# Kernel tuning notes

Hardware: AMD Instinct MI355X
Metric: run time of the kernel (lower is better)

Reference implementation:

```python
import jax, jax.numpy as jnp
import numpy as np

BATCH = 256
SEQ_LEN = 96
PRED_LEN = 96
ENC_IN = 321
D_MODEL = 512


def setup_inputs() -> dict:
    key = jax.random.key(0)
    ks = jax.random.split(key, 7)
    s = 1.0 / np.sqrt(D_MODEL)
    x_enc = jax.random.normal(ks[0], (BATCH, SEQ_LEN, ENC_IN), jnp.float32)
    Wih = jax.random.uniform(ks[1], (4 * D_MODEL, ENC_IN), jnp.float32, -s, s)
    Whh = jax.random.uniform(ks[2], (4 * D_MODEL, D_MODEL), jnp.float32, -s, s)
    bih = jax.random.uniform(ks[3], (4 * D_MODEL,), jnp.float32, -s, s)
    bhh = jax.random.uniform(ks[4], (4 * D_MODEL,), jnp.float32, -s, s)
    Wp = jax.random.uniform(ks[5], (ENC_IN, D_MODEL), jnp.float32, -s, s)
    bp = jax.random.uniform(ks[6], (ENC_IN,), jnp.float32, -s, s)
    return {"x_enc": x_enc, "Wih": Wih, "Whh": Whh, "bih": bih, "bhh": bhh, "Wp": Wp, "bp": bp}


def _lstm_step(h, c, xt, Wih, Whh, bih, bhh):
    # PyTorch LSTM gate layout: [i, f, g, o]
    g = xt @ Wih.T + h @ Whh.T + (bih + bhh)  # (B, 4*D)
    i, f, gg, o = jnp.split(g, 4, axis=-1)
    c = jax.nn.sigmoid(f) * c + jax.nn.sigmoid(i) * jnp.tanh(gg)
    h = jax.nn.sigmoid(o) * jnp.tanh(c)
    return h, c


def reference(x_enc, Wih, Whh, bih, bhh, Wp, bp):
    # Instance norm over time (use_norm=True); means detached as in torch
    means = jax.lax.stop_gradient(jnp.mean(x_enc, axis=1, keepdims=True))
    xc = x_enc - means
    stdev = jnp.sqrt(jnp.var(xc, axis=1, keepdims=True) + 1e-5)
    x = xc / stdev

    B = x.shape[0]
    h0 = jnp.zeros((B, D_MODEL), x.dtype)
    c0 = jnp.zeros((B, D_MODEL), x.dtype)

    def enc_step(carry, xt):
        h, c = carry
        h, c = _lstm_step(h, c, xt, Wih, Whh, bih, bhh)
        return (h, c), None

    (h, c), _ = jax.lax.scan(enc_step, (h0, c0), jnp.swapaxes(x, 0, 1))

    def dec_step(carry, _):
        h, c = carry
        y = h @ Wp.T + bp          # (B, ENC_IN) decoded from hidden
        h, c = _lstm_step(h, c, y, Wih, Whh, bih, bhh)
        return (h, c), y

    _, ys = jax.lax.scan(dec_step, (h, c), None, length=PRED_LEN)
    dec_out = jnp.swapaxes(ys, 0, 1)  # (B, PRED_LEN, ENC_IN)

    dec_out = dec_out * stdev[:, 0:1, :] + means[:, 0:1, :]
    return dec_out
```

## Files before the change

kernel.cpp:

```cpp
#include <hip/hip_runtime.h>
#include <hip/hip_bf16.h>
#include <math.h>

#define BB 256
#define TT 96
#define PP 96
#define CC 321
#define CP 352
#define DD 512
#define GG 2048
#define NSTEPS 191

typedef __attribute__((ext_vector_type(8))) short bf16x8;
typedef __attribute__((ext_vector_type(4))) float f32x4;
typedef __hip_bfloat16 bf16;
typedef unsigned long long u64;

__global__ void norm_kernel(const float* __restrict__ x, float* __restrict__ meanp,
                            float* __restrict__ stdp, bf16* __restrict__ xn) {
    int g = blockIdx.x * 256 + threadIdx.x;
    if (g >= BB * CC) return;
    int b = g / CC, c = g % CC;
    const float* xp = x + b * TT * CC + c;
    float s = 0.f;
    for (int t = 0; t < TT; ++t) s += xp[t * CC];
    float mu = s * (1.f / TT);
    float v = 0.f;
    for (int t = 0; t < TT; ++t) { float d0 = xp[t * CC] - mu; v += d0 * d0; }
    float sd = sqrtf(v * (1.f / TT) + 1e-5f);
    float rs = 1.f / sd;
    meanp[g] = mu;
    stdp[g] = sd;
    for (int t = 0; t < TT; ++t)
        xn[(t * BB + b) * CP + c] = __float2bfloat16((xp[t * CC] - mu) * rs);
}

__global__ void cast_pad_kernel(const float* __restrict__ src, bf16* __restrict__ dst,
                                int rows, int cols, int ldd) {
    int i = blockIdx.x * 256 + threadIdx.x;
    if (i >= rows * cols) return;
    int r = i / cols, c = i % cols;
    dst[r * ldd + c] = __float2bfloat16(src[i]);
}

__global__ void transpose_wp_kernel(const float* __restrict__ wp, bf16* __restrict__ wpt) {
    int i = blockIdx.x * 256 + threadIdx.x;
    if (i >= DD * CC) return;
    int d = i / CC, c = i % CC;
    wpt[d * CP + c] = __float2bfloat16(wp[c * DD + d]);
}

__global__ void bias_kernel(const float* __restrict__ Wih, const float* __restrict__ bih,
                            const float* __restrict__ bhh, const float* __restrict__ bp,
                            float* __restrict__ bsum, float* __restrict__ beff) {
    int j = blockIdx.x * 256 + threadIdx.x;
    if (j >= GG) return;
    float s = bih[j] + bhh[j];
    float acc = 0.f;
    const float* w = Wih + j * CC;
    for (int c = 0; c < CC; ++c) acc += w[c] * bp[c];
    bsum[j] = s;
    beff[j] = s + acc;
}

__device__ __forceinline__ void gemm_core_64x64(const bf16* A, int lda, const bf16* Bt,
                                                int ldb, int K, int m0, int n0,
                                                f32x4 acc[4]) {
    __shared__ unsigned short As[64][40];
    __shared__ unsigned short Bs[64][40];
    int tid = threadIdx.x;
    int w = tid >> 6, lane = tid & 63;
    int quad = lane >> 4, col = lane & 15;
    int lr = tid >> 2, lc = (tid & 3) * 8;
    for (int k0 = 0; k0 < K; k0 += 32) {
        __syncthreads();
        *(uint4*)&As[lr][lc] = *(const uint4*)&A[(size_t)(m0 + lr) * lda + k0 + lc];
        *(uint4*)&Bs[lr][lc] = *(const uint4*)&Bt[(size_t)(n0 + lr) * ldb + k0 + lc];
        __syncthreads();
        bf16x8 a = *(const bf16x8*)&As[w * 16 + col][quad * 8];
#pragma unroll
        for (int nt = 0; nt < 4; ++nt) {
            bf16x8 bfr = *(const bf16x8*)&Bs[nt * 16 + col][quad * 8];
            acc[nt] = __builtin_amdgcn_mfma_f32_16x16x32_bf16(a, bfr, acc[nt], 0, 0, 0);
        }
    }
}

__global__ void weff_kernel(const bf16* __restrict__ WihP, const bf16* __restrict__ WpTP,
                            const float* __restrict__ Whh, bf16* __restrict__ WeffP) {
    f32x4 acc[4] = {{0,0,0,0},{0,0,0,0},{0,0,0,0},{0,0,0,0}};
    int m0 = blockIdx.y * 64, n0 = blockIdx.x * 64;
    gemm_core_64x64(WihP, CP, WpTP, CP, CP, m0, n0, acc);
    int tid = threadIdx.x, w = tid >> 6, lane = tid & 63;
    int quad = lane >> 4, col = lane & 15;
#pragma unroll
    for (int nt = 0; nt < 4; ++nt)
#pragma unroll
        for (int r = 0; r < 4; ++r) {
            int j = m0 + w * 16 + quad * 4 + r;
            int d = n0 + nt * 16 + col;
            WeffP[j * DD + d] = __float2bfloat16(acc[nt][r] + Whh[j * DD + d]);
        }
}

__global__ void proj_kernel(const bf16* __restrict__ Hdec, const bf16* __restrict__ WpP,
                            const float* __restrict__ bp, const float* __restrict__ stdp,
                            const float* __restrict__ meanp, float* __restrict__ out) {
    f32x4 acc[4] = {{0,0,0,0},{0,0,0,0},{0,0,0,0},{0,0,0,0}};
    int m0 = blockIdx.x * 64, n0 = blockIdx.y * 64;
    gemm_core_64x64(Hdec, DD, WpP, DD, DD, m0, n0, acc);
    int tid = threadIdx.x, w = tid >> 6, lane = tid & 63;
    int quad = lane >> 4, col = lane & 15;
#pragma unroll
    for (int nt = 0; nt < 4; ++nt) {
        int c = n0 + nt * 16 + col;
        if (c >= CC) continue;
        float bpc = bp[c];
#pragma unroll
        for (int r = 0; r < 4; ++r) {
            int row = m0 + w * 16 + quad * 4 + r;
            int t = row >> 8, b = row & 255;
            float y = acc[nt][r] + bpc;
            int sc = b * CC + c;
            out[(b * PP + t) * CC + c] = y * stdp[sc] + meanp[sc];
        }
    }
}

__global__ __launch_bounds__(128, 1) void lstm_persistent(
        const bf16* __restrict__ xn,
        const bf16* __restrict__ WihP,
        const bf16* __restrict__ WhhP,
        const bf16* __restrict__ WeffP,
        const float* __restrict__ bsum, const float* __restrict__ beff,
        bf16* __restrict__ hA, bf16* __restrict__ hB,
        bf16* __restrict__ Hdec,
        unsigned int* __restrict__ bar) {
    __shared__ unsigned short Whs[4 * 16 * 64 * 8];
    __shared__ unsigned short Wxs[4 * 11 * 64 * 8];
    __shared__ int role_sh;

    const int tid = threadIdx.x;
    const int w = tid >> 6, lane = tid & 63;
    const int quad = lane >> 4, col = lane & 15;

    unsigned int xcd;
    asm volatile("s_getreg_b32 %0, hwreg(HW_REG_XCC_ID)" : "=s"(xcd));
    xcd &= 7;
    if (tid == 0)
        role_sh = (int)__hip_atomic_fetch_add(&bar[xcd], 1u, __ATOMIC_RELAXED,
                                              __HIP_MEMORY_SCOPE_AGENT);
    __syncthreads();
    const int dt = role_sh & 31;
    const int bt = (int)xcd;
    const int d0 = dt * 16;
    const int b0 = bt * 32;
    const int batch = b0 + w * 16 + col;
    unsigned int* const flags = bar + 64 + bt * 64;

    for (int i = tid; i < 4096; i += 128) {
        int q = i & 3, ki = (i >> 2) & 15, row = (i >> 6) & 15, gt = i >> 10;
        *(uint4*)&Whs[((gt * 16 + ki) * 64 + q * 16 + row) * 8] =
            *(const uint4*)&WhhP[(size_t)(gt * DD + d0 + row) * DD + ki * 32 + q * 8];
    }
    for (int i = tid; i < 2816; i += 128) {
        int q = i & 3; int t = i >> 2; int ki = t % 11; t /= 11;
        int row = t & 15, gt = t >> 4;
        *(uint4*)&Wxs[((gt * 11 + ki) * 64 + q * 16 + row) * 8] =
            *(const uint4*)&WihP[(size_t)(gt * DD + d0 + row) * CP + ki * 32 + q * 8];
    }
    __syncthreads();

    float creg[4] = {0.f, 0.f, 0.f, 0.f};
    float bs_[16], be_[16];
#pragma unroll
    for (int g4 = 0; g4 < 16; ++g4) {
        int gt = g4 >> 2, r = g4 & 3;
        bs_[g4] = bsum[gt * DD + d0 + quad * 4 + r];
        be_[g4] = beff[gt * DD + d0 + quad * 4 + r];
    }

    for (int s = 0; s < NSTEPS; ++s) {
        const bool enc = (s < TT);
        const bf16* h_in;
        bf16* h_out;
        if (enc) {
            h_in  = (s & 1) ? hB : hA;
            h_out = (s == TT - 1) ? Hdec : ((s & 1) ? hA : hB);
        } else {
            int td = s - TT;
            h_in  = Hdec + (size_t)td * BB * DD;
            h_out = Hdec + (size_t)(td + 1) * BB * DD;
        }

        f32x4 acc[4] = {{0,0,0,0},{0,0,0,0},{0,0,0,0},{0,0,0,0}};

        if (enc) {
            uint4 xf[11];
            const uint4* xp = (const uint4*)(xn + (size_t)(s * BB + batch) * CP) + quad;
#pragma unroll
            for (int ki = 0; ki < 11; ++ki) xf[ki] = xp[ki * 4];
#pragma unroll
            for (int ki = 0; ki < 11; ++ki) {
                bf16x8 xv = *(bf16x8*)&xf[ki];
#pragma unroll
                for (int gt = 0; gt < 4; ++gt) {
                    bf16x8 wf = *(const bf16x8*)&Wxs[((gt * 11 + ki) * 64 + lane) * 8];
                    acc[gt] = __builtin_amdgcn_mfma_f32_16x16x32_bf16(wf, xv, acc[gt], 0, 0, 0);
                }
            }
        }

        if (s > 0) {
            unsigned int tgt = (unsigned int)s;
            unsigned int v;
            int guard = 0;
            do {
                v = __hip_atomic_load(&flags[lane], __ATOMIC_RELAXED,
                                      __HIP_MEMORY_SCOPE_AGENT);
            } while (v < tgt && ++guard < (1 << 22));
            __builtin_amdgcn_sched_barrier(0);
        }

        if (s == TT) {
            for (int i = tid; i < 4096; i += 128) {
                int q = i & 3, ki = (i >> 2) & 15, row = (i >> 6) & 15, gt = i >> 10;
                *(uint4*)&Whs[((gt * 16 + ki) * 64 + q * 16 + row) * 8] =
                    *(const uint4*)&WeffP[(size_t)(gt * DD + d0 + row) * DD + ki * 32 + q * 8];
            }
            __syncthreads();
        }

        u64 hf[32];
        {
            u64* hp = (u64*)(h_in + (size_t)batch * DD);
#pragma unroll
            for (int ki = 0; ki < 16; ++ki) {
                hf[2 * ki] = __hip_atomic_load(&hp[ki * 8 + quad * 2],
                                               __ATOMIC_RELAXED, __HIP_MEMORY_SCOPE_AGENT);
                hf[2 * ki + 1] = __hip_atomic_load(&hp[ki * 8 + quad * 2 + 1],
                                                   __ATOMIC_RELAXED, __HIP_MEMORY_SCOPE_AGENT);
            }
        }

#pragma unroll
        for (int ki = 0; ki < 16; ++ki) {
            union { u64 q[2]; bf16x8 v; } hu;
            hu.q[0] = hf[2 * ki];
            hu.q[1] = hf[2 * ki + 1];
#pragma unroll
            for (int gt = 0; gt < 4; ++gt) {
                bf16x8 wf = *(const bf16x8*)&Whs[((gt * 16 + ki) * 64 + lane) * 8];
                acc[gt] = __builtin_amdgcn_mfma_f32_16x16x32_bf16(wf, hu.v, acc[gt], 0, 0, 0);
            }
        }

        u64 pack = 0;
#pragma unroll
        for (int r = 0; r < 4; ++r) {
            float iv = acc[0][r] + (enc ? bs_[0 + r] : be_[0 + r]);
            float fv = acc[1][r] + (enc ? bs_[4 + r] : be_[4 + r]);
            float gv = acc[2][r] + (enc ? bs_[8 + r] : be_[8 + r]);
            float ov = acc[3][r] + (enc ? bs_[12 + r] : be_[12 + r]);
            float si = 1.f / (1.f + __expf(-iv));
            float sf = 1.f / (1.f + __expf(-fv));
            float so = 1.f / (1.f + __expf(-ov));
            float tg = tanhf(gv);
            float cc = sf * creg[r] + si * tg;
            creg[r] = cc;
            float hvv = so * tanhf(cc);
            union { bf16 h; unsigned short u; } cv;
            cv.h = __float2bfloat16(hvv);
            pack |= (u64)cv.u << (16 * r);
        }
        __hip_atomic_store((u64*)&h_out[(size_t)batch * DD + d0 + quad * 4], pack,
                           __ATOMIC_RELAXED, __HIP_MEMORY_SCOPE_AGENT);
        asm volatile("s_waitcnt vmcnt(0)" ::: "memory");
        if (lane == 0)
            __hip_atomic_store(&flags[dt * 2 + w], (unsigned int)(s + 1),
                               __ATOMIC_RELAXED, __HIP_MEMORY_SCOPE_AGENT);
    }
}

extern "C" void kernel_launch(void* const* d_in, const int* in_sizes, int n_in,
                              void* d_out, int out_size, void* d_ws, size_t ws_size,
                              hipStream_t stream) {
    (void)in_sizes; (void)n_in; (void)out_size;
    const float* x_enc = (const float*)d_in[0];
    const float* Wih   = (const float*)d_in[1];
    const float* Whh   = (const float*)d_in[2];
    const float* bih   = (const float*)d_in[3];
    const float* bhh   = (const float*)d_in[4];
    const float* Wp    = (const float*)d_in[5];
    const float* bp    = (const float*)d_in[6];
    float* out = (float*)d_out;

    char* ws = (char*)d_ws;
    size_t off = 0;
    float* meanp = (float*)(ws + off); off += (size_t)BB * CC * 4;
    float* stdp  = (float*)(ws + off); off += (size_t)BB * CC * 4;
    bf16* xnormP = (bf16*)(ws + off);  off += (size_t)TT * BB * CP * 2;
    bf16* WihP   = (bf16*)(ws + off);  off += (size_t)GG * CP * 2;
    bf16* WhhP   = (bf16*)(ws + off);  off += (size_t)GG * DD * 2;
    bf16* WeffP  = (bf16*)(ws + off);  off += (size_t)GG * DD * 2;
    bf16* WpTP   = (bf16*)(ws + off);  off += (size_t)DD * CP * 2;
    bf16* WpP    = (bf16*)(ws + off);  off += (size_t)384 * DD * 2;
    float* bsum  = (float*)(ws + off); off += (size_t)GG * 4;
    float* beff  = (float*)(ws + off); off += (size_t)GG * 4;
    bf16* hA     = (bf16*)(ws + off);  off += (size_t)BB * DD * 2;
    bf16* hB     = (bf16*)(ws + off);  off += (size_t)BB * DD * 2;
    bf16* Hdec   = (bf16*)(ws + off);  off += (size_t)PP * BB * DD * 2;
    unsigned int* bar = (unsigned int*)(ws + off); off += 4096;
    if (ws_size < off) return;

    hipMemsetAsync(xnormP, 0, (size_t)TT * BB * CP * 2, stream);
    hipMemsetAsync(WihP,   0, (size_t)GG * CP * 2, stream);
    hipMemsetAsync(WpTP,   0, (size_t)DD * CP * 2, stream);
    hipMemsetAsync(WpP,    0, (size_t)384 * DD * 2, stream);
    hipMemsetAsync(hA,     0, (size_t)BB * DD * 2, stream);
    hipMemsetAsync(bar,    0, 4096, stream);

    norm_kernel<<<(BB * CC + 255) / 256, 256, 0, stream>>>(x_enc, meanp, stdp, xnormP);
    cast_pad_kernel<<<(GG * CC + 255) / 256, 256, 0, stream>>>(Wih, WihP, GG, CC, CP);
    cast_pad_kernel<<<(GG * DD + 255) / 256, 256, 0, stream>>>(Whh, WhhP, GG, DD, DD);
    cast_pad_kernel<<<(CC * DD + 255) / 256, 256, 0, stream>>>(Wp, WpP, CC, DD, DD);
    transpose_wp_kernel<<<(DD * CC + 255) / 256, 256, 0, stream>>>(Wp, WpTP);
    bias_kernel<<<GG / 256, 256, 0, stream>>>(Wih, bih, bhh, bp, bsum, beff);
    weff_kernel<<<dim3(DD / 64, GG / 64), 256, 0, stream>>>(WihP, WpTP, Whh, WeffP);

    const bf16* xn_c = xnormP;  const bf16* wih_c = WihP;
    const bf16* whh_c = WhhP;   const bf16* weff_c = WeffP;
    const float* bs_c = bsum;   const float* be_c = beff;
    bf16* hA_c = hA; bf16* hB_c = hB; bf16* hd_c = Hdec; unsigned int* bar_c = bar;
    void* args[] = {&xn_c, &wih_c, &whh_c, &weff_c, &bs_c, &be_c,
                    &hA_c, &hB_c, &hd_c, &bar_c};
    hipLaunchCooperativeKernel((void*)lstm_persistent, dim3(256), dim3(128),
                               args, 0, stream);

    proj_kernel<<<dim3(PP * BB / 64, 384 / 64), 256, 0, stream>>>(
        Hdec, WpP, bp, stdp, meanp, out);
}
```

Baseline: 1.569 ms.

## Use per-step hidden-state buffers and sleep-based flag polling in persistent LSTM

Replaces the ping-pong hA/hB hidden-state buffers with a separate slot per timestep, so a block that runs ahead can never overwrite a buffer that slower blocks are still reading. This removes the write-after-read hazard and the hA zero-memset, and skips the recurrent matmul at step 0 since h0 is zero. The spin-wait now has each lane poll one flag with s_sleep backoff, which cuts polling traffic but may add wake-up latency. The workspace grows to hold all 191 hidden states.

```diff
diff --git a/kernel.cpp b/kernel.cpp
--- a/kernel.cpp
+++ b/kernel.cpp
@@ -10,6 +10,7 @@
 #define DD 512
 #define GG 2048
 #define NSTEPS 191
+#define HROT ((size_t)BB * DD)
 
 typedef __attribute__((ext_vector_type(8))) short bf16x8;
 typedef __attribute__((ext_vector_type(4))) float f32x4;
@@ -103,12 +104,12 @@
         }
 }
 
-__global__ void proj_kernel(const bf16* __restrict__ Hdec, const bf16* __restrict__ WpP,
+__global__ void proj_kernel(const bf16* __restrict__ Hd, const bf16* __restrict__ WpP,
                             const float* __restrict__ bp, const float* __restrict__ stdp,
                             const float* __restrict__ meanp, float* __restrict__ out) {
     f32x4 acc[4] = {{0,0,0,0},{0,0,0,0},{0,0,0,0},{0,0,0,0}};
     int m0 = blockIdx.x * 64, n0 = blockIdx.y * 64;
-    gemm_core_64x64(Hdec, DD, WpP, DD, DD, m0, n0, acc);
+    gemm_core_64x64(Hd, DD, WpP, DD, DD, m0, n0, acc);
     int tid = threadIdx.x, w = tid >> 6, lane = tid & 63;
     int quad = lane >> 4, col = lane & 15;
 #pragma unroll
@@ -133,8 +134,7 @@
         const bf16* __restrict__ WhhP,
         const bf16* __restrict__ WeffP,
         const float* __restrict__ bsum, const float* __restrict__ beff,
-        bf16* __restrict__ hA, bf16* __restrict__ hB,
-        bf16* __restrict__ Hdec,
+        bf16* __restrict__ Hall,
         unsigned int* __restrict__ bar) {
     __shared__ unsigned short Whs[4 * 16 * 64 * 8];
     __shared__ unsigned short Wxs[4 * 11 * 64 * 8];
@@ -180,18 +180,12 @@
         be_[g4] = beff[gt * DD + d0 + quad * 4 + r];
     }
 
+    const size_t own_slot = (size_t)batch * DD + d0 + quad * 4;
+    const int fidx = (lane & 31) * 2 + w;
+
     for (int s = 0; s < NSTEPS; ++s) {
         const bool enc = (s < TT);
-        const bf16* h_in;
-        bf16* h_out;
-        if (enc) {
-            h_in  = (s & 1) ? hB : hA;
-            h_out = (s == TT - 1) ? Hdec : ((s & 1) ? hA : hB);
-        } else {
-            int td = s - TT;
-            h_in  = Hdec + (size_t)td * BB * DD;
-            h_out = Hdec + (size_t)(td + 1) * BB * DD;
-        }
+        bf16* h_out = Hall + (size_t)s * HROT;
 
         f32x4 acc[4] = {{0,0,0,0},{0,0,0,0},{0,0,0,0},{0,0,0,0}};
 
@@ -213,16 +207,17 @@
 
         if (s > 0) {
             unsigned int tgt = (unsigned int)s;
-            unsigned int v;
             int guard = 0;
-            do {
-                v = __hip_atomic_load(&flags[lane], __ATOMIC_RELAXED,
-                                      __HIP_MEMORY_SCOPE_AGENT);
-            } while (v < tgt && ++guard < (1 << 22));
+            while (__hip_atomic_load(&flags[fidx], __ATOMIC_RELAXED,
+                                     __HIP_MEMORY_SCOPE_AGENT) < tgt) {
+                __builtin_amdgcn_s_sleep(2);
+                if (++guard >= (1 << 20)) break;
+            }
             __builtin_amdgcn_sched_barrier(0);
         }
 
         if (s == TT) {
+            __syncthreads();
             for (int i = tid; i < 4096; i += 128) {
                 int q = i & 3, ki = (i >> 2) & 15, row = (i >> 6) & 15, gt = i >> 10;
                 *(uint4*)&Whs[((gt * 16 + ki) * 64 + q * 16 + row) * 8] =
@@ -231,9 +226,10 @@
             __syncthreads();
         }
 
-        u64 hf[32];
-        {
-            u64* hp = (u64*)(h_in + (size_t)batch * DD);
+        if (s > 0) {
+            u64 hf[32];
+            const u64* hp = (const u64*)(Hall + (size_t)(s - 1) * HROT
+                                         + (size_t)batch * DD);
 #pragma unroll
             for (int ki = 0; ki < 16; ++ki) {
                 hf[2 * ki] = __hip_atomic_load(&hp[ki * 8 + quad * 2],
@@ -241,17 +237,16 @@
                 hf[2 * ki + 1] = __hip_atomic_load(&hp[ki * 8 + quad * 2 + 1],
                                                    __ATOMIC_RELAXED, __HIP_MEMORY_SCOPE_AGENT);
             }
-        }
-
-#pragma unroll
-        for (int ki = 0; ki < 16; ++ki) {
-            union { u64 q[2]; bf16x8 v; } hu;
-            hu.q[0] = hf[2 * ki];
-            hu.q[1] = hf[2 * ki + 1];
-#pragma unroll
-            for (int gt = 0; gt < 4; ++gt) {
-                bf16x8 wf = *(const bf16x8*)&Whs[((gt * 16 + ki) * 64 + lane) * 8];
-                acc[gt] = __builtin_amdgcn_mfma_f32_16x16x32_bf16(wf, hu.v, acc[gt], 0, 0, 0);
+#pragma unroll
+            for (int ki = 0; ki < 16; ++ki) {
+                union { u64 q[2]; bf16x8 v; } hu;
+                hu.q[0] = hf[2 * ki];
+                hu.q[1] = hf[2 * ki + 1];
+#pragma unroll
+                for (int gt = 0; gt < 4; ++gt) {
+                    bf16x8 wf = *(const bf16x8*)&Whs[((gt * 16 + ki) * 64 + lane) * 8];
+                    acc[gt] = __builtin_amdgcn_mfma_f32_16x16x32_bf16(wf, hu.v, acc[gt], 0, 0, 0);
+                }
             }
         }
 
@@ -273,7 +268,7 @@
             cv.h = __float2bfloat16(hvv);
             pack |= (u64)cv.u << (16 * r);
         }
-        __hip_atomic_store((u64*)&h_out[(size_t)batch * DD + d0 + quad * 4], pack,
+        __hip_atomic_store((u64*)&h_out[own_slot], pack,
                            __ATOMIC_RELAXED, __HIP_MEMORY_SCOPE_AGENT);
         asm volatile("s_waitcnt vmcnt(0)" ::: "memory");
         if (lane == 0)
@@ -307,9 +302,7 @@
     bf16* WpP    = (bf16*)(ws + off);  off += (size_t)384 * DD * 2;
     float* bsum  = (float*)(ws + off); off += (size_t)GG * 4;
     float* beff  = (float*)(ws + off); off += (size_t)GG * 4;
-    bf16* hA     = (bf16*)(ws + off);  off += (size_t)BB * DD * 2;
-    bf16* hB     = (bf16*)(ws + off);  off += (size_t)BB * DD * 2;
-    bf16* Hdec   = (bf16*)(ws + off);  off += (size_t)PP * BB * DD * 2;
+    bf16* Hall   = (bf16*)(ws + off);  off += (size_t)NSTEPS * HROT * 2;
     unsigned int* bar = (unsigned int*)(ws + off); off += 4096;
     if (ws_size < off) return;
 
@@ -317,7 +310,6 @@
     hipMemsetAsync(WihP,   0, (size_t)GG * CP * 2, stream);
     hipMemsetAsync(WpTP,   0, (size_t)DD * CP * 2, stream);
     hipMemsetAsync(WpP,    0, (size_t)384 * DD * 2, stream);
-    hipMemsetAsync(hA,     0, (size_t)BB * DD * 2, stream);
     hipMemsetAsync(bar,    0, 4096, stream);
 
     norm_kernel<<<(BB * CC + 255) / 256, 256, 0, stream>>>(x_enc, meanp, stdp, xnormP);
@@ -331,12 +323,12 @@
     const bf16* xn_c = xnormP;  const bf16* wih_c = WihP;
     const bf16* whh_c = WhhP;   const bf16* weff_c = WeffP;
     const float* bs_c = bsum;   const float* be_c = beff;
-    bf16* hA_c = hA; bf16* hB_c = hB; bf16* hd_c = Hdec; unsigned int* bar_c = bar;
+    bf16* ha_c = Hall; unsigned int* bar_c = bar;
     void* args[] = {&xn_c, &wih_c, &whh_c, &weff_c, &bs_c, &be_c,
-                    &hA_c, &hB_c, &hd_c, &bar_c};
+                    &ha_c, &bar_c};
     hipLaunchCooperativeKernel((void*)lstm_persistent, dim3(256), dim3(128),
                                args, 0, stream);
 
     proj_kernel<<<dim3(PP * BB / 64, 384 / 64), 256, 0, stream>>>(
-        Hdec, WpP, bp, stdp, meanp, out);
-}
+        Hall + 95 * HROT, WpP, bp, stdp, meanp, out);
+}
```

After: 1.411 ms. 1.11x faster.
